# Kernel optimization log

Hardware: AMD Instinct MI355X
Metric: run time of the kernel (lower is better)

Reference implementation:

```python
import jax, jax.numpy as jnp
import numpy as np
from jax import lax

B, T, F, H, NC = 64, 256, 64, 128, 2


def setup_inputs() -> dict:
    key = jax.random.key(0)
    ks = jax.random.split(key, 10)
    # timestamps: sorted ints with duplicates -> exercises per-timestamp mean aggregation
    t = jnp.sort(jax.random.randint(ks[0], (B, T), 0, T // 2), axis=1).astype(jnp.float32)
    m = jax.random.randint(ks[1], (B, T), 0, F).astype(jnp.float32)
    x = jax.random.normal(ks[2], (B, T), dtype=jnp.float32)
    delt = jax.random.uniform(ks[3], (B, T), dtype=jnp.float32)
    X = jnp.stack([t, m, x, delt], axis=1)  # [B, 4, T]
    lengths = jax.random.randint(ks[4], (B,), T // 2, T + 1).astype(jnp.int32)
    s = 1.0 / np.sqrt(H + 1)
    W_lin = jax.random.uniform(ks[5], (F, H + 1, 4 * H), minval=-s, maxval=s, dtype=jnp.float32)
    b_lin = jax.random.uniform(ks[6], (F, 4 * H), minval=-s, maxval=s, dtype=jnp.float32)
    W_dec = jax.random.uniform(ks[7], (F,), minval=-1.0, maxval=1.0, dtype=jnp.float32)
    b_dec = jax.random.uniform(ks[8], (F,), minval=-1.0, maxval=1.0, dtype=jnp.float32)
    so = 1.0 / np.sqrt(F * H + H)
    k9, k10 = jax.random.split(ks[9])
    W_out = jax.random.uniform(k9, (F * H + H, NC), minval=-so, maxval=so, dtype=jnp.float32)
    b_out = jax.random.uniform(k10, (NC,), minval=-so, maxval=so, dtype=jnp.float32)
    return {"X": X, "lengths": lengths, "W_lin": W_lin, "b_lin": b_lin,
            "W_dec": W_dec, "b_dec": b_dec, "W_out": W_out, "b_out": b_out}


def _forward(X, lengths, W_lin, b_lin, W_dec, b_dec, W_out, b_out):
    nF, Hp1, H4 = W_lin.shape
    hs = Hp1 - 1
    t = X[:, 0]
    m = X[:, 1].astype(jnp.int32)
    x = X[:, 2]
    delt = X[:, 3]
    idx = jnp.arange(t.shape[1])
    valid = idx[None, :] < lengths[:, None]                       # event is real
    t_next = jnp.concatenate([t[:, 1:], t[:, -1:] + 1.0], axis=1)
    # last event of a consecutive-equal-timestamp group (within valid length)
    boundary = (idx[None, :] == (lengths[:, None] - 1)) | (t_next != t)

    def per_sample(m_s, x_s, d_s, v_s, b_s):
        def step(carry, inp):
            h_t, c_t, acc, cnt = carry
            mj, xj, dj, vj, bj = inp
            # feature-specific decay of that feature's hidden row
            dm = W_dec[mj] * dj + b_dec[mj]
            decay = jnp.exp(-jnp.maximum(0.0, dm))
            h_dec = decay * h_t[mj]
            inp_vec = jnp.concatenate([xj[None], h_dec])          # [H+1]
            gates = inp_vec @ W_lin[mj] + b_lin[mj]               # [4H]
            gi, gf, go, gc = jnp.split(gates, 4)
            c_cand = jax.nn.sigmoid(gf) * c_t + jax.nn.sigmoid(gi) * jnp.tanh(gc)
            h_row = jax.nn.sigmoid(go) * jnp.tanh(c_cand)
            h_t = jnp.where(vj, h_t.at[mj].set(h_row), h_t)
            acc = acc + jnp.where(vj, c_cand, 0.0)
            cnt = cnt + jnp.where(vj, 1.0, 0.0)
            close = vj & bj                                       # end of timestamp group
            c_t = jnp.where(close, acc / jnp.maximum(cnt, 1.0), c_t)
            acc = jnp.where(close, jnp.zeros_like(acc), acc)
            cnt = jnp.where(close, 0.0, cnt)
            return (h_t, c_t, acc, cnt), None

        init = (jnp.zeros((nF, hs), jnp.float32), jnp.zeros((hs,), jnp.float32),
                jnp.zeros((hs,), jnp.float32), jnp.float32(0.0))
        (h_t, c_t, _, _), _ = lax.scan(step, init, (m_s, x_s, d_s, v_s, b_s))
        feats = jnp.concatenate([c_t, h_t.reshape(-1)])           # [H + F*H]
        return jax.nn.softmax(feats @ W_out + b_out)

    return jax.vmap(per_sample)(m, x, delt, valid, boundary)      # [B, n_class]


def reference(X, lengths, W_lin, b_lin, W_dec, b_dec, W_out, b_out):
    return _forward(X, lengths, W_lin, b_lin, W_dec, b_dec, W_out, b_out)
```

## Files before the change

### kernel.cpp

```cpp
#include <hip/hip_runtime.h>
#include <math.h>
#include <stdint.h>

#define BATCH 64
#define T 256
#define NF 64
#define H 128
#define H4 512
#define HP1 129
#define WF_STRIDE (HP1 * H4)
#define FEATS (NF * H + H)
#define NTH 1024

#define RING_HALF 32768
#define PACK8_U4 (64 * 16 * 4 * 64)
#define PACK8_BYTES ((size_t)PACK8_U4 * 16u)
#define HDR_BYTES  (64u * 1024u * 2u)
#define WS_NEED ((size_t)HDR_BYTES + PACK8_BYTES)

typedef _Float16 half2_t __attribute__((ext_vector_type(2)));
typedef float    vf2     __attribute__((ext_vector_type(2)));

__device__ __forceinline__ float sigmoidf_(float x) {
    return 1.0f / (1.0f + __expf(-x));
}

__device__ __forceinline__ float tanhf_(float x) {
    float ax = fabsf(x);
    float e = __expf(2.0f * ax);
    float r = 1.0f - 2.0f / (e + 1.0f);
    return copysignf(r, x);
}

__device__ __forceinline__ float fdot2_(half2_t a, half2_t b, float c) {
#if defined(__has_builtin)
#if __has_builtin(__builtin_amdgcn_fdot2)
    return __builtin_amdgcn_fdot2(a, b, c, false);
#else
    return fmaf((float)a.x, (float)b.x, fmaf((float)a.y, (float)b.y, c));
#endif
#else
    return fmaf((float)a.x, (float)b.x, fmaf((float)a.y, (float)b.y, c));
#endif
}

template<bool HI>
__device__ __forceinline__ half2_t dec8(unsigned u) {
    vf2 f = __builtin_amdgcn_cvt_pk_f32_fp8(u, HI);
    return (half2_t)__builtin_amdgcn_cvt_pkrtz(f[0], f[1]);
}

__device__ __forceinline__ void dma16(const void* g, uint32_t lds_byte) {
    __builtin_amdgcn_global_load_lds(
        (const __attribute__((address_space(1))) void*)g,
        (__attribute__((address_space(3))) void*)(uintptr_t)lds_byte,
        16, 0, 0);
}
__device__ __forceinline__ void dma4(const void* g, uint32_t lds_byte) {
    __builtin_amdgcn_global_load_lds(
        (const __attribute__((address_space(1))) void*)g,
        (__attribute__((address_space(3))) void*)(uintptr_t)lds_byte,
        4, 0, 0);
}

#define WAITV(N) do { asm volatile("s_waitcnt vmcnt(" #N ")" ::: "memory"); \
                      __builtin_amdgcn_sched_barrier(0); } while (0)
#define BARRIER() do { asm volatile("s_waitcnt lgkmcnt(0)" ::: "memory"); \
                       __builtin_amdgcn_s_barrier(); \
                       asm volatile("" ::: "memory"); } while (0)

__global__ __launch_bounds__(256)
void repack8_kernel(const float* __restrict__ W_lin, uint4* __restrict__ pack) {
    const int lin = blockIdx.x * 256 + threadIdx.x;
    const int l   = lin & 63;
    const int i   = (lin >> 6) & 3;
    const int wv  = (lin >> 8) & 15;
    const int f   = lin >> 12;
    const int tid = wv * 64 + l;
    const int kh  = tid >> 9;
    const int cc  = tid & 511;
    const int k0  = kh * 64 + i * 16;
    unsigned u[4];
    #pragma unroll
    for (int w = 0; w < 4; ++w) {
        const float* src = W_lin + (size_t)f * WF_STRIDE + (size_t)(1 + k0 + 4 * w) * H4 + cc;
        const float v0 = src[0]      * 4096.0f;
        const float v1 = src[H4]     * 4096.0f;
        const float v2 = src[2 * H4] * 4096.0f;
        const float v3 = src[3 * H4] * 4096.0f;
        unsigned r = 0;
        r = __builtin_amdgcn_cvt_pk_fp8_f32(v0, v1, r, false);
        r = __builtin_amdgcn_cvt_pk_fp8_f32(v2, v3, r, true);
        u[w] = r;
    }
    uint4 o; o.x = u[0]; o.y = u[1]; o.z = u[2]; o.w = u[3];
    pack[lin] = o;
}

__global__ __launch_bounds__(256)
void hdr_kernel(const float* __restrict__ W_lin, const float* __restrict__ b_lin,
                _Float16* __restrict__ hdr) {
    const int lin = blockIdx.x * 256 + threadIdx.x;
    const int f = lin >> 10, t = lin & 1023;
    const float v = (t < 512) ? W_lin[(size_t)f * WF_STRIDE + t]
                              : b_lin[f * H4 + (t & 511)];
    hdr[lin] = (_Float16)v;
}

__global__ __launch_bounds__(NTH, 4)
void lstm_scan_fp8_dma(const float* __restrict__ X,
                       const int* __restrict__ lengths,
                       const float* __restrict__ W_dec,
                       const float* __restrict__ b_dec,
                       const float* __restrict__ W_out,
                       const float* __restrict__ b_out,
                       const uint4* __restrict__ pack,
                       const _Float16* __restrict__ hdr,
                       float* __restrict__ out)
{
    __shared__ __align__(16) char s_wb[3 * RING_HALF];
    __shared__ __align__(16) char s_hd[2 * 4096];
    __shared__ half2_t s_inp2[H / 2];
    __shared__ float s_ht[NF * H];
    __shared__ float s_part[2][H4];
    __shared__ float s_X[4 * T];
    __shared__ float s_wdec[NF];
    __shared__ float s_bdec[NF];
    __shared__ float s_cfin[H];
    __shared__ float s_red[32];

    const int tid  = threadIdx.x;
    const int b    = blockIdx.x;
    const int wv   = tid >> 6;
    const int lane = tid & 63;
    const int kh   = tid >> 9;
    const int c    = tid & 511;

    const float* Xb = X + b * 4 * T;
    const int len = lengths[b];

    for (int i = tid; i < NF * H; i += NTH) s_ht[i] = 0.0f;
    for (int i = tid; i < 4 * T; i += NTH) s_X[i] = Xb[i];
    if (tid < NF) { s_wdec[tid] = W_dec[tid]; s_bdec[tid] = b_dec[tid]; }
    if (tid < H) ((_Float16*)s_inp2)[tid] = (_Float16)0.0f;
    __syncthreads();

    const uint32_t wb0 = (uint32_t)(uintptr_t)s_wb;
    const uint32_t hd0 = (uint32_t)(uintptr_t)s_hd;
    const uint32_t wb_wave = __builtin_amdgcn_readfirstlane(wb0 + wv * 2048);
    const uint32_t hd_wave = __builtin_amdgcn_readfirstlane(hd0 + wv * 256);

    float c_t = 0.0f, acc = 0.0f, cnt = 0.0f;

    #define ISSUE_W(mf, i, slot) do {                                           \
        const uint4* gp = pack + (((size_t)(mf) * 16 + wv) * 4 + (i)) * 64 + lane; \
        dma16(gp, wb_wave + (uint32_t)(slot) * RING_HALF + ((i) & 1) * 1024);   \
    } while (0)

    #define ISSUE_HDR(jj) do {                                                  \
        const int ss = ((jj) < T) ? (jj) : (T - 1);                             \
        const _Float16* gh = hdr + (int)s_X[T + ss] * 1024 + (tid & 1022);      \
        dma4(gh, hd_wave + (((jj) & 1) ? 4096u : 0u));                          \
    } while (0)

    #define DOTU4(W, IB) do {                                                   \
        const half2_t* ip = ((const half2_t*)s_inp2) + (IB);                    \
        union { uint4 u; half2_t h[4]; } I0, I1;                                \
        I0.u = *(const uint4*)(ip);                                             \
        I1.u = *(const uint4*)(ip + 4);                                         \
        a0 = fdot2_(dec8<false>(W.x), I0.h[0], a0);                             \
        a1 = fdot2_(dec8<true >(W.x), I0.h[1], a1);                             \
        a0 = fdot2_(dec8<false>(W.y), I0.h[2], a0);                             \
        a1 = fdot2_(dec8<true >(W.y), I0.h[3], a1);                             \
        a0 = fdot2_(dec8<false>(W.z), I1.h[0], a0);                             \
        a1 = fdot2_(dec8<true >(W.z), I1.h[1], a1);                             \
        a0 = fdot2_(dec8<false>(W.w), I1.h[2], a0);                             \
        a1 = fdot2_(dec8<true >(W.w), I1.h[3], a1);                             \
    } while (0)

    #define HALF_DOT(slot, hh) do {                                             \
        const char* bp = s_wb + (size_t)(slot) * RING_HALF + wv * 2048 + lane * 16; \
        const uint4 W0 = *(const uint4*)(bp);                                   \
        const uint4 W1 = *(const uint4*)(bp + 1024);                            \
        DOTU4(W0, kh * 32 + 16 * (hh));                                         \
        DOTU4(W1, kh * 32 + 16 * (hh) + 8);                                     \
    } while (0)

    {
        const int m0 = (int)s_X[T];
        ISSUE_W(m0, 0, 0); ISSUE_W(m0, 1, 0);
        ISSUE_HDR(0);
        ISSUE_W(m0, 2, 1); ISSUE_W(m0, 3, 1);
    }

    int r0 = 0;
    for (int j = 0; j < len; ++j) {
        const int   mj  = (int)s_X[T + j];
        const float xj  = s_X[2 * T + j];
        const int   jn  = (j + 1 < T) ? (j + 1) : (T - 1);
        const int   mjn = (int)s_X[T + jn];
        int r1 = r0 + 1; if (r1 >= 3) r1 -= 3;
        int r2 = r0 + 2; if (r2 >= 3) r2 -= 3;

        ISSUE_W(mjn, 0, r2); ISSUE_W(mjn, 1, r2);
        ISSUE_HDR(j + 1);
        WAITV(5);

        float a0 = 0.0f, a1 = 0.0f;
        HALF_DOT(r0, 0);
        asm volatile("s_waitcnt lgkmcnt(0)" ::: "memory");
        __builtin_amdgcn_sched_barrier(0);
        ISSUE_W(mjn, 2, r0); ISSUE_W(mjn, 3, r0);
        WAITV(5);
        HALF_DOT(r1, 1);

        float a = (a0 + a1) * (1.0f / 4096.0f);
        {
            const float hv = (float)*(const _Float16*)(s_hd
                + ((j & 1) ? 4096 : 0) + wv * 256 + lane * 4 + (tid & 1) * 2);
            a = kh ? (a + hv) : fmaf(xj, hv, a);
        }
        s_part[kh][c] = a;
        BARRIER();

        if (tid < H) {
            const int h = tid;
            const float gi = s_part[0][h]         + s_part[1][h];
            const float gf = s_part[0][H + h]     + s_part[1][H + h];
            const float go = s_part[0][2 * H + h] + s_part[1][2 * H + h];
            const float gc = s_part[0][3 * H + h] + s_part[1][3 * H + h];
            const float c_cand = sigmoidf_(gf) * c_t + sigmoidf_(gi) * tanhf_(gc);
            const float h_row  = sigmoidf_(go) * tanhf_(c_cand);
            s_ht[mj * H + h] = h_row;
            acc += c_cand;
            cnt += 1.0f;
            const float tj = s_X[j];
            const float tn = (j < T - 1) ? s_X[j + 1] : (tj + 1.0f);
            const bool boundary = (j == len - 1) || (tn != tj);
            if (boundary) { c_t = acc / fmaxf(cnt, 1.0f); acc = 0.0f; cnt = 0.0f; }
            const float dn  = s_X[3 * T + jn];
            const float dmn = fmaf(s_wdec[mjn], dn, s_bdec[mjn]);
            const float den = __expf(-fmaxf(0.0f, dmn));
            const float hv2 = (mjn == mj) ? h_row : s_ht[mjn * H + h];
            ((_Float16*)s_inp2)[h] = (_Float16)(den * hv2);
        }
        BARRIER();
        r0 = r2;
    }
    #undef HALF_DOT
    #undef DOTU4
    #undef ISSUE_HDR
    #undef ISSUE_W

    asm volatile("s_waitcnt vmcnt(0) lgkmcnt(0)" ::: "memory");
    __syncthreads();

    if (tid < H) s_cfin[tid] = c_t;
    __syncthreads();

    float z0 = 0.0f, z1 = 0.0f;
    for (int i = tid; i < FEATS; i += NTH) {
        const float f = (i < H) ? s_cfin[i] : s_ht[i - H];
        const float2 w = *(const float2*)(W_out + 2 * i);
        z0 = fmaf(f, w.x, z0);
        z1 = fmaf(f, w.y, z1);
    }
    #pragma unroll
    for (int off = 32; off > 0; off >>= 1) {
        z0 += __shfl_down(z0, off, 64);
        z1 += __shfl_down(z1, off, 64);
    }
    const int wave = tid >> 6, lane2 = tid & 63;
    if (lane2 == 0) { s_red[2 * wave] = z0; s_red[2 * wave + 1] = z1; }
    __syncthreads();
    if (tid == 0) {
        float a0 = b_out[0], a1 = b_out[1];
        #pragma unroll
        for (int w = 0; w < 16; ++w) { a0 += s_red[2 * w]; a1 += s_red[2 * w + 1]; }
        const float mx = fmaxf(a0, a1);
        const float e0 = __expf(a0 - mx), e1 = __expf(a1 - mx);
        const float inv = 1.0f / (e0 + e1);
        out[2 * b]     = e0 * inv;
        out[2 * b + 1] = e1 * inv;
    }
}

#define NTHREADS 512
__global__ __launch_bounds__(NTHREADS)
void lstm_scan_kernel(const float* __restrict__ X,
                      const int* __restrict__ lengths,
                      const float* __restrict__ W_lin,
                      const float* __restrict__ b_lin,
                      const float* __restrict__ W_dec,
                      const float* __restrict__ b_dec,
                      const float* __restrict__ W_out,
                      const float* __restrict__ b_out,
                      float* __restrict__ out)
{
    __shared__ float s_feats[FEATS];
    __shared__ float s_inp[H];
    __shared__ float s_part[4][H4];
    __shared__ float s_X[4 * T];
    __shared__ float s_wdec[NF];
    __shared__ float s_bdec[NF];
    __shared__ float s_red[16];

    float* s_ct = s_feats;
    float* s_ht = s_feats + H;

    const int tid = threadIdx.x;
    const int b   = blockIdx.x;
    const int g4  = tid & 127;
    const int kq  = tid >> 7;

    const float* Xb = X + b * 4 * T;
    const int len = lengths[b];

    for (int i = tid; i < NF * H; i += NTHREADS) s_ht[i] = 0.0f;
    for (int i = tid; i < 4 * T; i += NTHREADS) s_X[i] = Xb[i];
    if (tid < NF) { s_wdec[tid] = W_dec[tid]; s_bdec[tid] = b_dec[tid]; }
    __syncthreads();

    float c_t = 0.0f, acc = 0.0f, cnt = 0.0f;

    for (int j = 0; j < len; ++j) {
        const int   mj = (int)s_X[T + j];
        const float xj = s_X[2 * T + j];
        const float* Wf = W_lin + mj * WF_STRIDE;

        float bl0, bl1, bl2, bl3;
        if (tid < H) {
            const float dj    = s_X[3 * T + j];
            const float dm    = fmaf(s_wdec[mj], dj, s_bdec[mj]);
            const float decay = __expf(-fmaxf(0.0f, dm));
            s_inp[tid] = decay * s_ht[mj * H + tid];
            const int m4 = mj * H4;
            bl0 = b_lin[m4 + tid];
            bl1 = b_lin[m4 + H + tid];
            bl2 = b_lin[m4 + 2 * H + tid];
            bl3 = b_lin[m4 + 3 * H + tid];
        }
        __syncthreads();

        float4 a4 = make_float4(0.0f, 0.0f, 0.0f, 0.0f);
        {
            const float*  wr  = Wf + (1 + kq * 32) * H4 + 4 * g4;
            const float4* ivp = (const float4*)(s_inp + kq * 32);
            #pragma unroll
            for (int cc = 0; cc < 8; ++cc) {
                const float4 v = ivp[cc];
                const float* wrc = wr + (4 * cc) * H4;
                const float4 w0 = *(const float4*)(wrc);
                const float4 w1 = *(const float4*)(wrc + H4);
                const float4 w2 = *(const float4*)(wrc + 2 * H4);
                const float4 w3 = *(const float4*)(wrc + 3 * H4);
                a4.x = fmaf(v.x, w0.x, a4.x); a4.y = fmaf(v.x, w0.y, a4.y);
                a4.z = fmaf(v.x, w0.z, a4.z); a4.w = fmaf(v.x, w0.w, a4.w);
                a4.x = fmaf(v.y, w1.x, a4.x); a4.y = fmaf(v.y, w1.y, a4.y);
                a4.z = fmaf(v.y, w1.z, a4.z); a4.w = fmaf(v.y, w1.w, a4.w);
                a4.x = fmaf(v.z, w2.x, a4.x); a4.y = fmaf(v.z, w2.y, a4.y);
                a4.z = fmaf(v.z, w2.z, a4.z); a4.w = fmaf(v.z, w2.w, a4.w);
                a4.x = fmaf(v.w, w3.x, a4.x); a4.y = fmaf(v.w, w3.y, a4.y);
                a4.z = fmaf(v.w, w3.z, a4.z); a4.w = fmaf(v.w, w3.w, a4.w);
            }
        }
        if (kq == 0) {
            const float4 w = *(const float4*)(Wf + 4 * g4);
            a4.x = fmaf(xj, w.x, a4.x); a4.y = fmaf(xj, w.y, a4.y);
            a4.z = fmaf(xj, w.z, a4.z); a4.w = fmaf(xj, w.w, a4.w);
        }
        *(float4*)(&s_part[kq][4 * g4]) = a4;
        __syncthreads();

        if (tid < H) {
            const int h = tid;
            const float gi = s_part[0][h]         + s_part[1][h]         + s_part[2][h]         + s_part[3][h]         + bl0;
            const float gf = s_part[0][H + h]     + s_part[1][H + h]     + s_part[2][H + h]     + s_part[3][H + h]     + bl1;
            const float go = s_part[0][2*H + h]   + s_part[1][2*H + h]   + s_part[2][2*H + h]   + s_part[3][2*H + h]   + bl2;
            const float gc = s_part[0][3*H + h]   + s_part[1][3*H + h]   + s_part[2][3*H + h]   + s_part[3][3*H + h]   + bl3;

            const float c_cand = sigmoidf_(gf) * c_t + sigmoidf_(gi) * tanhf_(gc);
            const float h_row  = sigmoidf_(go) * tanhf_(c_cand);
            s_ht[mj * H + h] = h_row;
            acc += c_cand;
            cnt += 1.0f;

            const float tj = s_X[j];
            const float tn = (j < T - 1) ? s_X[j + 1] : (tj + 1.0f);
            const bool boundary = (j == len - 1) || (tn != tj);
            if (boundary) { c_t = acc / fmaxf(cnt, 1.0f); acc = 0.0f; cnt = 0.0f; }
        }
        __syncthreads();
    }

    if (tid < H) s_ct[tid] = c_t;
    __syncthreads();

    float z0 = 0.0f, z1 = 0.0f;
    for (int i = tid; i < FEATS; i += NTHREADS) {
        const float f = s_feats[i];
        const float2 w = *(const float2*)(W_out + 2 * i);
        z0 = fmaf(f, w.x, z0);
        z1 = fmaf(f, w.y, z1);
    }
    #pragma unroll
    for (int off = 32; off > 0; off >>= 1) {
        z0 += __shfl_down(z0, off, 64);
        z1 += __shfl_down(z1, off, 64);
    }
    const int wave = tid >> 6, lane = tid & 63;
    if (lane == 0) { s_red[2 * wave] = z0; s_red[2 * wave + 1] = z1; }
    __syncthreads();
    if (tid == 0) {
        float a0 = b_out[0], a1 = b_out[1];
        #pragma unroll
        for (int w = 0; w < 8; ++w) { a0 += s_red[2 * w]; a1 += s_red[2 * w + 1]; }
        const float mx = fmaxf(a0, a1);
        const float e0 = __expf(a0 - mx), e1 = __expf(a1 - mx);
        const float inv = 1.0f / (e0 + e1);
        out[2 * b]     = e0 * inv;
        out[2 * b + 1] = e1 * inv;
    }
}

extern "C" void kernel_launch(void* const* d_in, const int* in_sizes, int n_in,
                              void* d_out, int out_size, void* d_ws, size_t ws_size,
                              hipStream_t stream) {
    const float* X      = (const float*)d_in[0];
    const int*   lens   = (const int*)d_in[1];
    const float* W_lin  = (const float*)d_in[2];
    const float* b_lin  = (const float*)d_in[3];
    const float* W_dec  = (const float*)d_in[4];
    const float* b_dec  = (const float*)d_in[5];
    const float* W_out  = (const float*)d_in[6];
    const float* b_out  = (const float*)d_in[7];
    float* out = (float*)d_out;

    if (ws_size >= WS_NEED) {
        _Float16* hdr = (_Float16*)d_ws;
        uint4* pack = (uint4*)((char*)d_ws + HDR_BYTES);
        hipLaunchKernelGGL(repack8_kernel, dim3(PACK8_U4 / 256), dim3(256), 0, stream,
                           W_lin, pack);
        hipLaunchKernelGGL(hdr_kernel, dim3(256), dim3(256), 0, stream, W_lin, b_lin, hdr);
        hipLaunchKernelGGL(lstm_scan_fp8_dma, dim3(BATCH), dim3(NTH), 0, stream,
                           X, lens, W_dec, b_dec, W_out, b_out, pack, hdr, out);
    } else {
        hipLaunchKernelGGL(lstm_scan_kernel, dim3(BATCH), dim3(NTHREADS), 0, stream,
                           X, lens, W_lin, b_lin, W_dec, b_dec, W_out, b_out, out);
    }
}
```

Baseline: 493.1 us.

## Restructure LSTM scan to 512 threads with per-wave gate ownership and shuffle reduction

The per-step recurrent matvec is remapped so each wave owns 16 hidden units across all four gates. The K reduction is split over 4 lane groups and finished with cross-lane shuffles, replacing the shared-memory partial sums and single-thread gate stage. The block shrinks from 1024 to 512 threads, and fp8 weights are decoded to f32 pairs and accumulated with packed float math instead of fp16 dot2. Gate math now runs redundantly in every lane group, but one barrier per timestep and the serial tid<H tail are removed; the weight and header repack layouts and DMA schedule change to match.

```diff
diff --git a/kernel.cpp b/kernel.cpp
--- a/kernel.cpp
+++ b/kernel.cpp
@@ -10,16 +10,15 @@
 #define HP1 129
 #define WF_STRIDE (HP1 * H4)
 #define FEATS (NF * H + H)
-#define NTH 1024
-
-#define RING_HALF 32768
-#define PACK8_U4 (64 * 16 * 4 * 64)
-#define PACK8_BYTES ((size_t)PACK8_U4 * 16u)
-#define HDR_BYTES  (64u * 1024u * 2u)
-#define WS_NEED ((size_t)HDR_BYTES + PACK8_BYTES)
-
-typedef _Float16 half2_t __attribute__((ext_vector_type(2)));
-typedef float    vf2     __attribute__((ext_vector_type(2)));
+#define NTH2 512
+
+#define RING_SLOT 32768
+#define PACK2_U4 (64 * 8 * 2 * 4 * 64)
+#define PACK2_BYTES ((size_t)PACK2_U4 * 16u)
+#define HDR2_BYTES  (64u * 512u * 16u)
+#define WS_NEED ((size_t)HDR2_BYTES + PACK2_BYTES)
+
+typedef float vf2 __attribute__((ext_vector_type(2)));
 
 __device__ __forceinline__ float sigmoidf_(float x) {
     return 1.0f / (1.0f + __expf(-x));
@@ -32,22 +31,9 @@
     return copysignf(r, x);
 }
 
-__device__ __forceinline__ float fdot2_(half2_t a, half2_t b, float c) {
-#if defined(__has_builtin)
-#if __has_builtin(__builtin_amdgcn_fdot2)
-    return __builtin_amdgcn_fdot2(a, b, c, false);
-#else
-    return fmaf((float)a.x, (float)b.x, fmaf((float)a.y, (float)b.y, c));
-#endif
-#else
-    return fmaf((float)a.x, (float)b.x, fmaf((float)a.y, (float)b.y, c));
-#endif
-}
-
 template<bool HI>
-__device__ __forceinline__ half2_t dec8(unsigned u) {
-    vf2 f = __builtin_amdgcn_cvt_pk_f32_fp8(u, HI);
-    return (half2_t)__builtin_amdgcn_cvt_pkrtz(f[0], f[1]);
+__device__ __forceinline__ vf2 dec2f(unsigned u) {
+    return __builtin_amdgcn_cvt_pk_f32_fp8(u, HI);
 }
 
 __device__ __forceinline__ void dma16(const void* g, uint32_t lds_byte) {
@@ -56,141 +42,158 @@
         (__attribute__((address_space(3))) void*)(uintptr_t)lds_byte,
         16, 0, 0);
 }
-__device__ __forceinline__ void dma4(const void* g, uint32_t lds_byte) {
-    __builtin_amdgcn_global_load_lds(
-        (const __attribute__((address_space(1))) void*)g,
-        (__attribute__((address_space(3))) void*)(uintptr_t)lds_byte,
-        4, 0, 0);
-}
 
 #define WAITV(N) do { asm volatile("s_waitcnt vmcnt(" #N ")" ::: "memory"); \
+                      __builtin_amdgcn_sched_barrier(0); } while (0)
+#define LGKM0()  do { asm volatile("s_waitcnt lgkmcnt(0)" ::: "memory"); \
                       __builtin_amdgcn_sched_barrier(0); } while (0)
 #define BARRIER() do { asm volatile("s_waitcnt lgkmcnt(0)" ::: "memory"); \
                        __builtin_amdgcn_s_barrier(); \
                        asm volatile("" ::: "memory"); } while (0)
 
 __global__ __launch_bounds__(256)
-void repack8_kernel(const float* __restrict__ W_lin, uint4* __restrict__ pack) {
+void repack2_kernel(const float* __restrict__ W_lin, uint4* __restrict__ pack2) {
     const int lin = blockIdx.x * 256 + threadIdx.x;
     const int l   = lin & 63;
     const int i   = (lin >> 6) & 3;
-    const int wv  = (lin >> 8) & 15;
+    const int Xv  = (lin >> 8) & 1;
+    const int wv  = (lin >> 9) & 7;
     const int f   = lin >> 12;
-    const int tid = wv * 64 + l;
-    const int kh  = tid >> 9;
-    const int cc  = tid & 511;
-    const int k0  = kh * 64 + i * 16;
+    const int h   = wv * 16 + (l & 15);
+    const int ks  = l >> 4;
+    const int g   = Xv * 2 + (i >> 1);
+    const int ksub = i & 1;
+    const int col = g * 128 + h;
+    const int k0  = ks * 32 + ksub * 16;
+    const float* src = W_lin + (size_t)f * WF_STRIDE + (size_t)(1 + k0) * H4 + col;
     unsigned u[4];
     #pragma unroll
-    for (int w = 0; w < 4; ++w) {
-        const float* src = W_lin + (size_t)f * WF_STRIDE + (size_t)(1 + k0 + 4 * w) * H4 + cc;
-        const float v0 = src[0]      * 4096.0f;
-        const float v1 = src[H4]     * 4096.0f;
-        const float v2 = src[2 * H4] * 4096.0f;
-        const float v3 = src[3 * H4] * 4096.0f;
+    for (int dw = 0; dw < 4; ++dw) {
+        const float v0 = src[(4 * dw + 0) * H4] * 4096.0f;
+        const float v1 = src[(4 * dw + 1) * H4] * 4096.0f;
+        const float v2 = src[(4 * dw + 2) * H4] * 4096.0f;
+        const float v3 = src[(4 * dw + 3) * H4] * 4096.0f;
         unsigned r = 0;
         r = __builtin_amdgcn_cvt_pk_fp8_f32(v0, v1, r, false);
         r = __builtin_amdgcn_cvt_pk_fp8_f32(v2, v3, r, true);
-        u[w] = r;
+        u[dw] = r;
     }
     uint4 o; o.x = u[0]; o.y = u[1]; o.z = u[2]; o.w = u[3];
-    pack[lin] = o;
+    pack2[lin] = o;
 }
 
 __global__ __launch_bounds__(256)
-void hdr_kernel(const float* __restrict__ W_lin, const float* __restrict__ b_lin,
-                _Float16* __restrict__ hdr) {
+void hdr2_kernel(const float* __restrict__ W_lin, const float* __restrict__ b_lin,
+                 uint4* __restrict__ hdr2) {
     const int lin = blockIdx.x * 256 + threadIdx.x;
-    const int f = lin >> 10, t = lin & 1023;
-    const float v = (t < 512) ? W_lin[(size_t)f * WF_STRIDE + t]
-                              : b_lin[f * H4 + (t & 511)];
-    hdr[lin] = (_Float16)v;
-}
-
-__global__ __launch_bounds__(NTH, 4)
-void lstm_scan_fp8_dma(const float* __restrict__ X,
-                       const int* __restrict__ lengths,
-                       const float* __restrict__ W_dec,
-                       const float* __restrict__ b_dec,
-                       const float* __restrict__ W_out,
-                       const float* __restrict__ b_out,
-                       const uint4* __restrict__ pack,
-                       const _Float16* __restrict__ hdr,
-                       float* __restrict__ out)
+    const int t2 = lin & 511, f = lin >> 9;
+    const int wv = t2 >> 6, l = t2 & 63;
+    const int h  = wv * 16 + (l & 15);
+    union { uint4 u; _Float16 hf[8]; } o;
+    #pragma unroll
+    for (int g = 0; g < 4; ++g) {
+        o.hf[g]     = (_Float16)W_lin[(size_t)f * WF_STRIDE + g * 128 + h];
+        o.hf[4 + g] = (_Float16)b_lin[f * H4 + g * 128 + h];
+    }
+    hdr2[lin] = o.u;
+}
+
+__global__ __launch_bounds__(NTH2)
+void lstm_scan_fp8_w1(const float* __restrict__ X,
+                      const int* __restrict__ lengths,
+                      const float* __restrict__ W_dec,
+                      const float* __restrict__ b_dec,
+                      const float* __restrict__ W_out,
+                      const float* __restrict__ b_out,
+                      const uint4* __restrict__ pack2,
+                      const uint4* __restrict__ hdr2,
+                      float* __restrict__ out)
 {
-    __shared__ __align__(16) char s_wb[3 * RING_HALF];
-    __shared__ __align__(16) char s_hd[2 * 4096];
-    __shared__ half2_t s_inp2[H / 2];
+    __shared__ __align__(16) char s_wb[3 * RING_SLOT];
+    __shared__ __align__(16) char s_hd[2 * 8192];
     __shared__ float s_ht[NF * H];
-    __shared__ float s_part[2][H4];
+    __shared__ float s_inp[H];
     __shared__ float s_X[4 * T];
     __shared__ float s_wdec[NF];
     __shared__ float s_bdec[NF];
     __shared__ float s_cfin[H];
-    __shared__ float s_red[32];
-
-    const int tid  = threadIdx.x;
-    const int b    = blockIdx.x;
-    const int wv   = tid >> 6;
-    const int lane = tid & 63;
-    const int kh   = tid >> 9;
-    const int c    = tid & 511;
+    __shared__ float s_red[16];
+
+    const int tid = threadIdx.x;
+    const int b   = blockIdx.x;
+    const int w   = tid >> 6;
+    const int l   = tid & 63;
+    const int h   = w * 16 + (l & 15);
+    const int ks  = l >> 4;
 
     const float* Xb = X + b * 4 * T;
     const int len = lengths[b];
 
-    for (int i = tid; i < NF * H; i += NTH) s_ht[i] = 0.0f;
-    for (int i = tid; i < 4 * T; i += NTH) s_X[i] = Xb[i];
+    for (int i = tid; i < NF * H; i += NTH2) s_ht[i] = 0.0f;
+    for (int i = tid; i < 4 * T; i += NTH2) s_X[i] = Xb[i];
     if (tid < NF) { s_wdec[tid] = W_dec[tid]; s_bdec[tid] = b_dec[tid]; }
-    if (tid < H) ((_Float16*)s_inp2)[tid] = (_Float16)0.0f;
+    if (tid < H) s_inp[tid] = 0.0f;
     __syncthreads();
 
     const uint32_t wb0 = (uint32_t)(uintptr_t)s_wb;
     const uint32_t hd0 = (uint32_t)(uintptr_t)s_hd;
-    const uint32_t wb_wave = __builtin_amdgcn_readfirstlane(wb0 + wv * 2048);
-    const uint32_t hd_wave = __builtin_amdgcn_readfirstlane(hd0 + wv * 256);
-
-    float c_t = 0.0f, acc = 0.0f, cnt = 0.0f;
-
-    #define ISSUE_W(mf, i, slot) do {                                           \
-        const uint4* gp = pack + (((size_t)(mf) * 16 + wv) * 4 + (i)) * 64 + lane; \
-        dma16(gp, wb_wave + (uint32_t)(slot) * RING_HALF + ((i) & 1) * 1024);   \
+    const uint32_t wbase  = __builtin_amdgcn_readfirstlane(wb0 + (uint32_t)w * 4096u);
+    const uint32_t hdbase = __builtin_amdgcn_readfirstlane(hd0 + (uint32_t)w * 1024u);
+
+    float c_t = 0.0f, accv = 0.0f, cntv = 0.0f;
+
+    #define ISSUE_W4(mf, Xv, slot) do {                                          \
+        const uint4* gp = pack2 + ((((size_t)(mf) * 8 + w) * 2 + (Xv)) * 4) * 64 + l; \
+        const uint32_t dst = wbase + (uint32_t)(slot) * RING_SLOT;               \
+        dma16(gp,       dst);                                                    \
+        dma16(gp + 64,  dst + 1024u);                                            \
+        dma16(gp + 128, dst + 2048u);                                            \
+        dma16(gp + 192, dst + 3072u);                                            \
     } while (0)
 
-    #define ISSUE_HDR(jj) do {                                                  \
-        const int ss = ((jj) < T) ? (jj) : (T - 1);                             \
-        const _Float16* gh = hdr + (int)s_X[T + ss] * 1024 + (tid & 1022);      \
-        dma4(gh, hd_wave + (((jj) & 1) ? 4096u : 0u));                          \
+    #define ISSUE_HDR(jj) do {                                                   \
+        const int ss = ((jj) < T) ? (jj) : (T - 1);                              \
+        const int mf = (int)s_X[T + ss];                                         \
+        const uint4* gh = hdr2 + (size_t)mf * 512 + (w * 64 + l);                \
+        dma16(gh, hdbase + (((jj) & 1) ? 8192u : 0u));                           \
     } while (0)
 
-    #define DOTU4(W, IB) do {                                                   \
-        const half2_t* ip = ((const half2_t*)s_inp2) + (IB);                    \
-        union { uint4 u; half2_t h[4]; } I0, I1;                                \
-        I0.u = *(const uint4*)(ip);                                             \
-        I1.u = *(const uint4*)(ip + 4);                                         \
-        a0 = fdot2_(dec8<false>(W.x), I0.h[0], a0);                             \
-        a1 = fdot2_(dec8<true >(W.x), I0.h[1], a1);                             \
-        a0 = fdot2_(dec8<false>(W.y), I0.h[2], a0);                             \
-        a1 = fdot2_(dec8<true >(W.y), I0.h[3], a1);                             \
-        a0 = fdot2_(dec8<false>(W.z), I1.h[0], a0);                             \
-        a1 = fdot2_(dec8<true >(W.z), I1.h[1], a1);                             \
-        a0 = fdot2_(dec8<false>(W.w), I1.h[2], a0);                             \
-        a1 = fdot2_(dec8<true >(W.w), I1.h[3], a1);                             \
+    #define DOTQ(Wq, G, KS) do {                                                 \
+        const int pb = (KS) * 8;                                                 \
+        vf2 d;                                                                   \
+        d = dec2f<false>((Wq).x); acc[G] += d * iv[pb + 0];                      \
+        d = dec2f<true >((Wq).x); acc[G] += d * iv[pb + 1];                      \
+        d = dec2f<false>((Wq).y); acc[G] += d * iv[pb + 2];                      \
+        d = dec2f<true >((Wq).y); acc[G] += d * iv[pb + 3];                      \
+        d = dec2f<false>((Wq).z); acc[G] += d * iv[pb + 4];                      \
+        d = dec2f<true >((Wq).z); acc[G] += d * iv[pb + 5];                      \
+        d = dec2f<false>((Wq).w); acc[G] += d * iv[pb + 6];                      \
+        d = dec2f<true >((Wq).w); acc[G] += d * iv[pb + 7];                      \
     } while (0)
 
-    #define HALF_DOT(slot, hh) do {                                             \
-        const char* bp = s_wb + (size_t)(slot) * RING_HALF + wv * 2048 + lane * 16; \
-        const uint4 W0 = *(const uint4*)(bp);                                   \
-        const uint4 W1 = *(const uint4*)(bp + 1024);                            \
-        DOTU4(W0, kh * 32 + 16 * (hh));                                         \
-        DOTU4(W1, kh * 32 + 16 * (hh) + 8);                                     \
+    #define HALFX(Xv, slot) do {                                                 \
+        uint4 q0, q1, q2, q3;                                                    \
+        const uint32_t ra = wb0 + (uint32_t)(slot) * RING_SLOT                   \
+                          + (uint32_t)w * 4096u + (uint32_t)l * 16u;             \
+        asm volatile("ds_read_b128 %0, %4 offset:0\n\t"                          \
+                     "ds_read_b128 %1, %4 offset:1024\n\t"                       \
+                     "ds_read_b128 %2, %4 offset:2048\n\t"                       \
+                     "ds_read_b128 %3, %4 offset:3072"                           \
+                     : "=&v"(q0), "=&v"(q1), "=&v"(q2), "=&v"(q3)                \
+                     : "v"(ra) : "memory");                                      \
+        asm volatile("s_waitcnt lgkmcnt(0)" ::: "memory");                       \
+        __builtin_amdgcn_sched_barrier(0);                                       \
+        DOTQ(q0, (Xv) * 2 + 0, 0);                                               \
+        DOTQ(q1, (Xv) * 2 + 0, 1);                                               \
+        DOTQ(q2, (Xv) * 2 + 1, 0);                                               \
+        DOTQ(q3, (Xv) * 2 + 1, 1);                                               \
     } while (0)
 
     {
         const int m0 = (int)s_X[T];
-        ISSUE_W(m0, 0, 0); ISSUE_W(m0, 1, 0);
+        ISSUE_W4(m0, 0, 0);
         ISSUE_HDR(0);
-        ISSUE_W(m0, 2, 1); ISSUE_W(m0, 3, 1);
+        ISSUE_W4(m0, 1, 1);
     }
 
     int r0 = 0;
@@ -202,81 +205,95 @@
         int r1 = r0 + 1; if (r1 >= 3) r1 -= 3;
         int r2 = r0 + 2; if (r2 >= 3) r2 -= 3;
 
-        ISSUE_W(mjn, 0, r2); ISSUE_W(mjn, 1, r2);
+        ISSUE_W4(mjn, 0, r2);
         ISSUE_HDR(j + 1);
-        WAITV(5);
-
-        float a0 = 0.0f, a1 = 0.0f;
-        HALF_DOT(r0, 0);
-        asm volatile("s_waitcnt lgkmcnt(0)" ::: "memory");
-        __builtin_amdgcn_sched_barrier(0);
-        ISSUE_W(mjn, 2, r0); ISSUE_W(mjn, 3, r0);
-        WAITV(5);
-        HALF_DOT(r1, 1);
-
-        float a = (a0 + a1) * (1.0f / 4096.0f);
+
+        vf2 iv[16];
         {
-            const float hv = (float)*(const _Float16*)(s_hd
-                + ((j & 1) ? 4096 : 0) + wv * 256 + lane * 4 + (tid & 1) * 2);
-            a = kh ? (a + hv) : fmaf(xj, hv, a);
-        }
-        s_part[kh][c] = a;
-        BARRIER();
-
-        if (tid < H) {
-            const int h = tid;
-            const float gi = s_part[0][h]         + s_part[1][h];
-            const float gf = s_part[0][H + h]     + s_part[1][H + h];
-            const float go = s_part[0][2 * H + h] + s_part[1][2 * H + h];
-            const float gc = s_part[0][3 * H + h] + s_part[1][3 * H + h];
-            const float c_cand = sigmoidf_(gf) * c_t + sigmoidf_(gi) * tanhf_(gc);
-            const float h_row  = sigmoidf_(go) * tanhf_(c_cand);
+            const float4* ip = (const float4*)(s_inp + ks * 32);
+            #pragma unroll
+            for (int q = 0; q < 8; ++q) {
+                const float4 t = ip[q];
+                iv[2 * q][0] = t.x;  iv[2 * q][1] = t.y;
+                iv[2 * q + 1][0] = t.z; iv[2 * q + 1][1] = t.w;
+            }
+        }
+        vf2 acc[4];
+        #pragma unroll
+        for (int g = 0; g < 4; ++g) { acc[g][0] = 0.0f; acc[g][1] = 0.0f; }
+
+        WAITV(9);
+        HALFX(0, r0);
+
+        uint4 hb;
+        {
+            const uint32_t ha = hd0 + ((j & 1) ? 8192u : 0u)
+                              + (uint32_t)w * 1024u + (uint32_t)l * 16u;
+            asm volatile("ds_read_b128 %0, %1" : "=&v"(hb) : "v"(ha) : "memory");
+        }
+        LGKM0();
+        ISSUE_W4(mjn, 1, r0);
+        WAITV(9);
+        HALFX(1, r1);
+
+        union { uint4 u; _Float16 hf[8]; } hu; hu.u = hb;
+        float gate[4];
+        #pragma unroll
+        for (int g = 0; g < 4; ++g) {
+            float s = acc[g][0] + acc[g][1];
+            s += __shfl_xor(s, 16, 64);
+            s += __shfl_xor(s, 32, 64);
+            gate[g] = fmaf(s, 1.0f / 4096.0f,
+                           fmaf(xj, (float)hu.hf[g], (float)hu.hf[4 + g]));
+        }
+        const float c_cand = sigmoidf_(gate[1]) * c_t + sigmoidf_(gate[0]) * tanhf_(gate[3]);
+        const float h_row  = sigmoidf_(gate[2]) * tanhf_(c_cand);
+        accv += c_cand;
+        cntv += 1.0f;
+        const float tj = s_X[j];
+        const float tn = (j < T - 1) ? s_X[j + 1] : (tj + 1.0f);
+        const bool boundary = (j == len - 1) || (tn != tj);
+        if (boundary) { c_t = accv / fmaxf(cntv, 1.0f); accv = 0.0f; cntv = 0.0f; }
+        if ((l & 48) == 0) {
             s_ht[mj * H + h] = h_row;
-            acc += c_cand;
-            cnt += 1.0f;
-            const float tj = s_X[j];
-            const float tn = (j < T - 1) ? s_X[j + 1] : (tj + 1.0f);
-            const bool boundary = (j == len - 1) || (tn != tj);
-            if (boundary) { c_t = acc / fmaxf(cnt, 1.0f); acc = 0.0f; cnt = 0.0f; }
             const float dn  = s_X[3 * T + jn];
             const float dmn = fmaf(s_wdec[mjn], dn, s_bdec[mjn]);
             const float den = __expf(-fmaxf(0.0f, dmn));
-            const float hv2 = (mjn == mj) ? h_row : s_ht[mjn * H + h];
-            ((_Float16*)s_inp2)[h] = (_Float16)(den * hv2);
+            const float hv  = (mjn == mj) ? h_row : s_ht[mjn * H + h];
+            s_inp[h] = den * hv;
         }
         BARRIER();
         r0 = r2;
     }
-    #undef HALF_DOT
-    #undef DOTU4
+    #undef HALFX
+    #undef DOTQ
     #undef ISSUE_HDR
-    #undef ISSUE_W
+    #undef ISSUE_W4
 
     asm volatile("s_waitcnt vmcnt(0) lgkmcnt(0)" ::: "memory");
     __syncthreads();
 
-    if (tid < H) s_cfin[tid] = c_t;
+    if ((l & 48) == 0) s_cfin[h] = c_t;
     __syncthreads();
 
     float z0 = 0.0f, z1 = 0.0f;
-    for (int i = tid; i < FEATS; i += NTH) {
+    for (int i = tid; i < FEATS; i += NTH2) {
         const float f = (i < H) ? s_cfin[i] : s_ht[i - H];
-        const float2 w = *(const float2*)(W_out + 2 * i);
-        z0 = fmaf(f, w.x, z0);
-        z1 = fmaf(f, w.y, z1);
+        const float2 wo = *(const float2*)(W_out + 2 * i);
+        z0 = fmaf(f, wo.x, z0);
+        z1 = fmaf(f, wo.y, z1);
     }
     #pragma unroll
     for (int off = 32; off > 0; off >>= 1) {
         z0 += __shfl_down(z0, off, 64);
         z1 += __shfl_down(z1, off, 64);
     }
-    const int wave = tid >> 6, lane2 = tid & 63;
-    if (lane2 == 0) { s_red[2 * wave] = z0; s_red[2 * wave + 1] = z1; }
+    if (l == 0) { s_red[2 * w] = z0; s_red[2 * w + 1] = z1; }
     __syncthreads();
     if (tid == 0) {
         float a0 = b_out[0], a1 = b_out[1];
         #pragma unroll
-        for (int w = 0; w < 16; ++w) { a0 += s_red[2 * w]; a1 += s_red[2 * w + 1]; }
+        for (int q = 0; q < 8; ++q) { a0 += s_red[2 * q]; a1 += s_red[2 * q + 1]; }
         const float mx = fmaxf(a0, a1);
         const float e0 = __expf(a0 - mx), e1 = __expf(a1 - mx);
         const float inv = 1.0f / (e0 + e1);
@@ -365,9 +382,9 @@
             }
         }
         if (kq == 0) {
-            const float4 w = *(const float4*)(Wf + 4 * g4);
-            a4.x = fmaf(xj, w.x, a4.x); a4.y = fmaf(xj, w.y, a4.y);
-            a4.z = fmaf(xj, w.z, a4.z); a4.w = fmaf(xj, w.w, a4.w);
+            const float4 wv = *(const float4*)(Wf + 4 * g4);
+            a4.x = fmaf(xj, wv.x, a4.x); a4.y = fmaf(xj, wv.y, a4.y);
+            a4.z = fmaf(xj, wv.z, a4.z); a4.w = fmaf(xj, wv.w, a4.w);
         }
         *(float4*)(&s_part[kq][4 * g4]) = a4;
         __syncthreads();
@@ -399,9 +416,9 @@
     float z0 = 0.0f, z1 = 0.0f;
     for (int i = tid; i < FEATS; i += NTHREADS) {
         const float f = s_feats[i];
-        const float2 w = *(const float2*)(W_out + 2 * i);
-        z0 = fmaf(f, w.x, z0);
-        z1 = fmaf(f, w.y, z1);
+        const float2 wv = *(const float2*)(W_out + 2 * i);
+        z0 = fmaf(f, wv.x, z0);
+        z1 = fmaf(f, wv.y, z1);
     }
     #pragma unroll
     for (int off = 32; off > 0; off >>= 1) {
@@ -414,7 +431,7 @@
     if (tid == 0) {
         float a0 = b_out[0], a1 = b_out[1];
         #pragma unroll
-        for (int w = 0; w < 8; ++w) { a0 += s_red[2 * w]; a1 += s_red[2 * w + 1]; }
+        for (int q = 0; q < 8; ++q) { a0 += s_red[2 * q]; a1 += s_red[2 * q + 1]; }
         const float mx = fmaxf(a0, a1);
         const float e0 = __expf(a0 - mx), e1 = __expf(a1 - mx);
         const float inv = 1.0f / (e0 + e1);
@@ -437,13 +454,14 @@
     float* out = (float*)d_out;
 
     if (ws_size >= WS_NEED) {
-        _Float16* hdr = (_Float16*)d_ws;
-        uint4* pack = (uint4*)((char*)d_ws + HDR_BYTES);
-        hipLaunchKernelGGL(repack8_kernel, dim3(PACK8_U4 / 256), dim3(256), 0, stream,
-                           W_lin, pack);
-        hipLaunchKernelGGL(hdr_kernel, dim3(256), dim3(256), 0, stream, W_lin, b_lin, hdr);
-        hipLaunchKernelGGL(lstm_scan_fp8_dma, dim3(BATCH), dim3(NTH), 0, stream,
-                           X, lens, W_dec, b_dec, W_out, b_out, pack, hdr, out);
+        uint4* hdr2 = (uint4*)d_ws;
+        uint4* pack2 = (uint4*)((char*)d_ws + HDR2_BYTES);
+        hipLaunchKernelGGL(hdr2_kernel, dim3(128), dim3(256), 0, stream,
+                           W_lin, b_lin, hdr2);
+        hipLaunchKernelGGL(repack2_kernel, dim3(PACK2_U4 / 256), dim3(256), 0, stream,
+                           W_lin, pack2);
+        hipLaunchKernelGGL(lstm_scan_fp8_w1, dim3(BATCH), dim3(NTH2), 0, stream,
+                           X, lens, W_dec, b_dec, W_out, b_out, pack2, hdr2, out);
     } else {
         hipLaunchKernelGGL(lstm_scan_kernel, dim3(BATCH), dim3(NTHREADS), 0, stream,
                            X, lens, W_lin, b_lin, W_dec, b_dec, W_out, b_out, out);
```

Result: slower. 507.6 us (+2.9%).
